# Kernel optimization log

Measured on AMD Instinct MI355X. Metric: run time of the kernel, lower is better.

Reference implementation:

```python
import jax, jax.numpy as jnp
import numpy as np

B = 4096          # batch
N_SPARSE = 26     # sparse fields (inputs[:,13:])
N_DENSE = 13      # dense fields (sliced off but unused in original forward)
VOCAB = 100000
EMB = 16
N_PAIRS = N_SPARSE * (N_SPARSE - 1) // 2  # 325


def setup_inputs() -> dict:
    key = jax.random.key(0)
    ks = jax.random.split(key, 8)
    return {
        "dense_x": jax.random.normal(ks[0], (B, N_DENSE), dtype=jnp.float32),
        "sparse_ids": jax.random.randint(ks[1], (B, N_SPARSE), 0, VOCAB, dtype=jnp.int32),
        "embed_tables": jax.random.normal(ks[2], (N_SPARSE, VOCAB, EMB), dtype=jnp.float32) * 0.05,
        "attn_w_kernel": jax.random.normal(ks[3], (EMB, N_PAIRS), dtype=jnp.float32) * (1.0 / np.sqrt(EMB)),
        "attn_w_bias": jnp.zeros((N_PAIRS,), dtype=jnp.float32),
        "attn_h_kernel": jax.random.normal(ks[4], (N_PAIRS, 1), dtype=jnp.float32) * (1.0 / np.sqrt(N_PAIRS)),
        "attn_h_bias": jnp.zeros((1,), dtype=jnp.float32),
        "out_kernel": jax.random.normal(ks[5], (1, 1), dtype=jnp.float32),
        "out_bias": jnp.zeros((1,), dtype=jnp.float32),
    }


def reference(dense_x, sparse_ids, embed_tables, attn_w_kernel, attn_w_bias,
              attn_h_kernel, attn_h_bias, out_kernel, out_bias):
    # Per-field embedding lookup: [B, 26, EMB]
    emb = embed_tables[jnp.arange(N_SPARSE), sparse_ids]
    # Pairwise elementwise interaction in the original double-loop order
    ii, jj = np.triu_indices(N_SPARSE, k=1)      # 325 (i<j) pairs, row-major
    pair = emb[:, ii, :] * emb[:, jj, :]          # [B, 325, EMB]
    # Attention net: Dense(325, relu) -> Dense(1) -> softmax over LAST axis.
    # Faithful to the original: softmax over an axis of size 1 yields all-ones.
    h = jax.nn.relu(jnp.einsum('bpe,ef->bpf', pair, attn_w_kernel) + attn_w_bias)  # [B,325,325]
    s = jnp.einsum('bpf,fo->bpo', h, attn_h_kernel) + attn_h_bias                  # [B,325,1]
    a = jax.nn.softmax(s, axis=-1)                                                 # [B,325,1] (== 1.0)
    # a^T @ pair : [B,1,325]@[B,325,EMB] -> [B,EMB]
    pooled = jnp.einsum('bpo,bpe->be', a, pair)
    x = jnp.sum(pooled, axis=1, keepdims=True)   # [B,1]
    return jax.nn.sigmoid(x @ out_kernel + out_bias)  # [B,1]
```

## Files before the change

kernel.cpp:

```cpp
#include <hip/hip_runtime.h>
#include <hip/hip_bf16.h>
#include <math.h>


#define B_ROWS 4096
#define N_SPARSE 26
#define VOCAB 100000
#define EMB 16

__global__ __launch_bounds__(256) void AFM_6700148981883_kernel(
    const int* __restrict__ ids,
    const float* __restrict__ tables,
    const float* __restrict__ out_k,
    const float* __restrict__ out_b,
    float* __restrict__ out)
{
    int tid = blockIdx.x * blockDim.x + threadIdx.x;
    int row = tid >> 4;
    int e   = tid & 15;
    if (row >= B_ROWS) return;

    const int* rid = ids + row * N_SPARSE;

    float s = 0.0f, sq = 0.0f;
#pragma unroll
    for (int i = 0; i < N_SPARSE; ++i) {
        int id = rid[i];
        float v = tables[((size_t)i * VOCAB + (size_t)id) * EMB + e];
        s  += v;
        sq += v * v;
    }

    float x = 0.5f * (s * s - sq);

    x += __shfl_xor(x, 8, 16);
    x += __shfl_xor(x, 4, 16);
    x += __shfl_xor(x, 2, 16);
    x += __shfl_xor(x, 1, 16);

    if (e == 0) {
        float z = x * out_k[0] + out_b[0];
        out[row] = 1.0f / (1.0f + expf(-z));
    }
}

extern "C" void kernel_launch(void* const* d_in, const int* in_sizes, int n_in,
                              void* d_out, int out_size, void* d_ws, size_t ws_size,
                              hipStream_t stream) {
    const int*   ids    = (const int*)  d_in[1];
    const float* tables = (const float*)d_in[2];
    const float* out_k  = (const float*)d_in[7];
    const float* out_b  = (const float*)d_in[8];
    float* out = (float*)d_out;

    const int threads = B_ROWS * 16;
    const int block = 256;
    AFM_6700148981883_kernel<<<(threads + block - 1) / block, block, 0, stream>>>(
        ids, tables, out_k, out_b, out);
}
```

Before: 212.2 us.

## Split field gathers across four lane groups per row with wave-level reduction

Each row is now handled by a full 64-lane wavefront instead of 16 lanes. The 26 fields are split into four partitions of six or seven fields, and ids are loaded once per lane and broadcast with shuffles. The aim is more memory-level parallelism for the random embedding gathers, with shorter dependent chains per thread. The cost is four times as many threads, extra cross-lane shuffle reductions, and a reworked sum-of-squares algebra that assumes s is reduced across all four groups.

```diff
diff --git a/kernel.cpp b/kernel.cpp
--- a/kernel.cpp
+++ b/kernel.cpp
@@ -8,6 +8,8 @@
 #define VOCAB 100000
 #define EMB 16
 
+__device__ __constant__ int kPartStart[5] = {0, 7, 14, 20, 26};
+
 __global__ __launch_bounds__(256) void AFM_6700148981883_kernel(
     const int* __restrict__ ids,
     const float* __restrict__ tables,
@@ -15,31 +17,40 @@
     const float* __restrict__ out_b,
     float* __restrict__ out)
 {
-    int tid = blockIdx.x * blockDim.x + threadIdx.x;
-    int row = tid >> 4;
-    int e   = tid & 15;
-    if (row >= B_ROWS) return;
+    int tid  = blockIdx.x * blockDim.x + threadIdx.x;
+    int row  = tid >> 6;
+    int t    = tid & 63;
+    int e    = t & 15;
+    int part = t >> 4;
 
     const int* rid = ids + row * N_SPARSE;
+    int myid = (t < N_SPARSE) ? rid[t] : 0;
+
+    int f0 = kPartStart[part];
+    int f1 = kPartStart[part + 1];
 
     float s = 0.0f, sq = 0.0f;
-#pragma unroll
-    for (int i = 0; i < N_SPARSE; ++i) {
-        int id = rid[i];
-        float v = tables[((size_t)i * VOCAB + (size_t)id) * EMB + e];
+#pragma unroll 7
+    for (int f = f0; f < f1; ++f) {
+        int id = __shfl(myid, f, 64);
+        float v = tables[((size_t)f * VOCAB + (size_t)id) * EMB + e];
         s  += v;
         sq += v * v;
     }
 
-    float x = 0.5f * (s * s - sq);
+    s += __shfl_xor(s, 16, 64);
+    s += __shfl_xor(s, 32, 64);
+    float y = 0.125f * s * s - 0.5f * sq;
 
-    x += __shfl_xor(x, 8, 16);
-    x += __shfl_xor(x, 4, 16);
-    x += __shfl_xor(x, 2, 16);
-    x += __shfl_xor(x, 1, 16);
+    y += __shfl_xor(y, 1, 64);
+    y += __shfl_xor(y, 2, 64);
+    y += __shfl_xor(y, 4, 64);
+    y += __shfl_xor(y, 8, 64);
+    y += __shfl_xor(y, 16, 64);
+    y += __shfl_xor(y, 32, 64);
 
-    if (e == 0) {
-        float z = x * out_k[0] + out_b[0];
+    if (t == 0) {
+        float z = y * out_k[0] + out_b[0];
         out[row] = 1.0f / (1.0f + expf(-z));
     }
 }
@@ -53,7 +64,7 @@
     const float* out_b  = (const float*)d_in[8];
     float* out = (float*)d_out;
 
-    const int threads = B_ROWS * 16;
+    const int threads = B_ROWS * 64;
     const int block = 256;
     AFM_6700148981883_kernel<<<(threads + block - 1) / block, block, 0, stream>>>(
         ids, tables, out_k, out_b, out);
```

Result: no change. 211.4 us (-0.4%).
